# Performance work log

Hardware: AMD Instinct MI355X
Metric: run time of the kernel (lower is better)

## Reference

```python
import jax, jax.numpy as jnp
import numpy as np

D_TOTAL, H, D_HEAD, HID = 2048, 16, 128, 512
EPS = float(np.finfo(np.float32).eps)  # nn.RMSNorm eps=None -> dtype eps


def _xavier(key, shape):
    # xavier_uniform over last two dims (per-head init)
    fan_in, fan_out = shape[-2], shape[-1]
    limit = float(np.sqrt(6.0 / (fan_in + fan_out)))
    return jax.random.uniform(key, shape, jnp.float32, -limit, limit)


def setup_inputs() -> dict:
    key = jax.random.key(0)
    ks = jax.random.split(key, 6)
    x = jax.random.normal(ks[0], (4, 4096, D_TOTAL), jnp.float32)
    g = jnp.ones((D_TOTAL,), jnp.float32)  # RMSNorm weight
    w0 = _xavier(ks[1], (H, D_HEAD, HID))
    w1 = _xavier(ks[2], (H, HID, HID))
    w2 = _xavier(ks[3], (H, HID, HID))
    w3 = _xavier(ks[4], (H, HID, D_HEAD))
    return {"x": x, "g": g, "w0": w0, "w1": w1, "w2": w2, "w3": w3}


def _rms_norm(x, g):
    var = jnp.mean(jnp.square(x), axis=-1, keepdims=True)
    return x * jax.lax.rsqrt(var + EPS) * g


def reference(x, g, w0, w1, w2, w3):
    h = _rms_norm(x, g)
    lead = h.shape[:-1]
    hp = h.reshape(*lead, H, D_HEAD)  # (B,S,H,d_head)
    gelu = lambda t: jax.nn.gelu(t, approximate=False)
    hp = jnp.einsum('bshd,hde->bshe', hp, w0)
    hp = jnp.einsum('bshd,hde->bshe', gelu(hp), w1)
    hp = jnp.einsum('bshd,hde->bshe', gelu(hp), w2)
    hp = jnp.einsum('bshd,hde->bshe', gelu(hp), w3)
    return hp.reshape(*lead, D_TOTAL)
```

## Files before the change

kernel.cpp:

```cpp
#include <hip/hip_runtime.h>
#include <cstdint>
#include <cstddef>

#define N_TOK   16384
#define D_TOTAL 2048
#define N_HEAD  16
#define D_HEAD  128
#define HID     512
#define MT      64
#define RMS_EPS 1.1920929e-07f

typedef __attribute__((ext_vector_type(8))) short  short8;
typedef __attribute__((ext_vector_type(4))) float  float4_t;
typedef __attribute__((ext_vector_type(2))) unsigned int uint2_t;

__device__ __forceinline__ unsigned short f2bf(float f) {
    union { float f; unsigned int i; } v; v.f = f;
    unsigned int b = v.i;
    b += 0x7FFFu + ((b >> 16) & 1u);
    return (unsigned short)(b >> 16);
}

__device__ __forceinline__ unsigned int cvt_pk_bf16(float lo, float hi) {
    unsigned int r;
    asm("v_cvt_pk_bf16_f32 %0, %1, %2" : "=v"(r) : "v"(lo), "v"(hi));
    return r;
}

__device__ __forceinline__ float gelu_exact(float x) {
    float ax = fabsf(x);
    float t  = __builtin_amdgcn_rcpf(fmaf(0.23164193f, ax, 1.0f));
    float poly = fmaf(fmaf(fmaf(fmaf(1.061405429f, t, -1.453152027f),
                               t, 1.421413741f), t, -0.284496736f),
                      t, 0.254829592f) * t;
    float e    = exp2f(x * x * -0.72134752f);
    float erfa = fmaf(-poly, e, 1.0f);
    return fmaf(0.5f * ax, erfa, 0.5f * x);
}

__global__ __launch_bounds__(256) void rms_scale_kernel(
    const float* __restrict__ x, float* __restrict__ scale)
{
    const int lane  = threadIdx.x & 63;
    const int wv    = threadIdx.x >> 6;
    const int token = blockIdx.x * 4 + wv;

    const float* xp = x + (size_t)token * D_TOTAL;
    float s = 0.0f;
#pragma unroll
    for (int j = 0; j < 8; ++j) {
        float4 v = *(const float4*)(xp + (size_t)(j * 64 + lane) * 4);
        s += v.x * v.x + v.y * v.y + v.z * v.z + v.w * v.w;
    }
#pragma unroll
    for (int off = 32; off > 0; off >>= 1) s += __shfl_down(s, off, 64);
    if (lane == 0)
        scale[token] = rsqrtf(s * (1.0f / (float)D_TOTAL) + RMS_EPS);
}

__global__ __launch_bounds__(256) void transpose_kernel(
    const float* __restrict__ in, unsigned short* __restrict__ out, int K, int N,
    const float* __restrict__ gmul)
{
    const int ktiles = K >> 6, ntiles = N >> 6;
    const int b   = blockIdx.x;
    const int h   = b / (ktiles * ntiles);
    const int rem = b % (ktiles * ntiles);
    const int kt  = rem / ntiles, nt = rem % ntiles;

    const float* src = in + (size_t)h * K * N + (size_t)(kt * 64) * N + nt * 64;
    unsigned short* dst = out + (size_t)h * N * K + (size_t)(nt * 64) * K + kt * 64;

    __shared__ unsigned short tile[64][72];

#pragma unroll
    for (int p = 0; p < 2; ++p) {
        int gi = threadIdx.x + p * 256;
        int r  = gi >> 3;
        int gc = (gi & 7) * 8;
        float mul = 1.0f;
        if (gmul) mul = gmul[(size_t)h * K + kt * 64 + r];
        float4 a  = *(const float4*)(src + (size_t)r * N + gc);
        float4 b4 = *(const float4*)(src + (size_t)r * N + gc + 4);
        unsigned short tmp[8];
        tmp[0]=f2bf(a.x*mul);  tmp[1]=f2bf(a.y*mul);  tmp[2]=f2bf(a.z*mul);  tmp[3]=f2bf(a.w*mul);
        tmp[4]=f2bf(b4.x*mul); tmp[5]=f2bf(b4.y*mul); tmp[6]=f2bf(b4.z*mul); tmp[7]=f2bf(b4.w*mul);
        *(uint4*)&tile[r][gc] = *(const uint4*)tmp;
    }
    __syncthreads();
#pragma unroll
    for (int p = 0; p < 2; ++p) {
        int gi  = threadIdx.x + p * 256;
        int r2  = gi >> 3;
        int gc2 = (gi & 7) * 8;
        unsigned short tmp[8];
#pragma unroll
        for (int j = 0; j < 8; ++j) tmp[j] = tile[gc2 + j][r2];
        *(uint4*)(dst + (size_t)r2 * K + gc2) = *(const uint4*)tmp;
    }
}

template<int K, int NT>
__device__ __forceinline__ void stage_gemm(
    const unsigned short* __restrict__ sA,
    const unsigned short* __restrict__ wt,
    int lane, int nbase, float4_t acc[4][NT])
{
#pragma unroll
    for (int mt = 0; mt < 4; ++mt)
#pragma unroll
        for (int nt = 0; nt < NT; ++nt) {
            float4_t z = {0.0f, 0.0f, 0.0f, 0.0f};
            acc[mt][nt] = z;
        }

    const int r15 = lane & 15;
    const int q   = lane >> 4;

    const char* arow[NT];
#pragma unroll
    for (int nt = 0; nt < NT; ++nt)
        arow[nt] = (const char*)(wt + (size_t)(nbase + nt * 16 + r15) * K + q * 8);

    const char* sab = (const char*)sA;
    unsigned int vb[4];
    const unsigned int hb = ((unsigned)(r15 >> 2) & 1u) << 6;
#pragma unroll
    for (int mt = 0; mt < 4; ++mt) {
        unsigned int row = (unsigned)(mt * 16 + r15);
        vb[mt] = row * 1024u + (((unsigned)(q ^ (r15 & 3))) << 4) + hb;
    }

#pragma unroll
    for (int ks = 0; ks < K / 32; ++ks) {
        short8 a[NT], b[4];
#pragma unroll
        for (int nt = 0; nt < NT; ++nt)
            a[nt] = *(const short8*)(arow[nt] + ks * 64);
#pragma unroll
        for (int mt = 0; mt < 4; ++mt)
            b[mt] = *(const short8*)(sab + (vb[mt] ^ (unsigned)(ks * 64)));
#pragma unroll
        for (int mt = 0; mt < 4; ++mt)
#pragma unroll
            for (int nt = 0; nt < NT; ++nt)
                acc[mt][nt] = __builtin_amdgcn_mfma_f32_16x16x32_bf16(
                    a[nt], b[mt], acc[mt][nt], 0, 0, 0);
    }
}

template<int NT>
__device__ __forceinline__ void epi_gelu(
    unsigned short* __restrict__ sAct, int lane, int nbase, float4_t acc[4][NT])
{
    const int q  = lane >> 4;
    const int c0 = lane & 15;
#pragma unroll
    for (int mt = 0; mt < 4; ++mt) {
        const int tok   = mt * 16 + c0;
        const unsigned int rbase = (unsigned)tok * HID;
        const int tk7   = tok & 7;
#pragma unroll
        for (int nt = 0; nt < NT; ++nt) {
            const int col = nbase + nt * 16 + q * 4;
            float g0 = gelu_exact(acc[mt][nt][0]);
            float g1 = gelu_exact(acc[mt][nt][1]);
            float g2 = gelu_exact(acc[mt][nt][2]);
            float g3 = gelu_exact(acc[mt][nt][3]);
            uint2_t v;
            v.x = cvt_pk_bf16(g0, g1);
            v.y = cvt_pk_bf16(g2, g3);
            const int gsw = (col >> 3) ^ tk7;
            *(uint2_t*)&sAct[rbase + gsw * 8 + (col & 7)] = v;
        }
    }
}

__global__ __launch_bounds__(512, 4) void fused_chain_kernel(
    const float*          __restrict__ x,
    const float*          __restrict__ scale,
    const unsigned short* __restrict__ wt0,
    const unsigned short* __restrict__ wt1,
    const unsigned short* __restrict__ wt2,
    const unsigned short* __restrict__ wt3,
    float*                __restrict__ out)
{
    __shared__ unsigned short sAct[MT * HID];

    const int tid  = threadIdx.x;
    const int lane = tid & 63;
    const int wv   = tid >> 6;
    const int bx    = blockIdx.x;
    const int xcd   = bx & 7;
    const int local = bx >> 3;
    const int head  = xcd * 2 + (local >> 8);
    const int tile  = local & 255;
    const int tok0  = tile * MT;

#pragma unroll
    for (int p = 0; p < 2; ++p) {
        int gi = tid + p * 512;
        int r  = gi >> 4;
        int gc = gi & 15;
        int token = tok0 + r;
        const float* xp = x + (size_t)token * D_TOTAL + head * D_HEAD + gc * 8;
        float4 xa = *(const float4*)(xp);
        float4 xb = *(const float4*)(xp + 4);
        float s = scale[token];
        unsigned int u[4];
        u[0] = cvt_pk_bf16(xa.x * s, xa.y * s);
        u[1] = cvt_pk_bf16(xa.z * s, xa.w * s);
        u[2] = cvt_pk_bf16(xb.x * s, xb.y * s);
        u[3] = cvt_pk_bf16(xb.z * s, xb.w * s);
        int gsw = gc ^ (r & 7);
        *(uint4*)&sAct[r * HID + gsw * 8] = *(const uint4*)u;
    }
    __syncthreads();

    float4_t acc[4][4];
    const int nb = wv * 64;

    stage_gemm<128, 4>(sAct, wt0 + (size_t)head * HID * D_HEAD, lane, nb, acc);
    __syncthreads();
    epi_gelu<4>(sAct, lane, nb, acc);
    __syncthreads();

    stage_gemm<512, 4>(sAct, wt1 + (size_t)head * HID * HID, lane, nb, acc);
    __syncthreads();
    epi_gelu<4>(sAct, lane, nb, acc);
    __syncthreads();

    stage_gemm<512, 4>(sAct, wt2 + (size_t)head * HID * HID, lane, nb, acc);
    __syncthreads();
    epi_gelu<4>(sAct, lane, nb, acc);
    __syncthreads();

    float4_t acc2[4][1];
    stage_gemm<512, 1>(sAct, wt3 + (size_t)head * D_HEAD * HID, lane, wv * 16, acc2);

    const int q  = lane >> 4;
    const int c0 = lane & 15;
#pragma unroll
    for (int mt = 0; mt < 4; ++mt) {
        const int token = tok0 + mt * 16 + c0;
        const int col   = head * D_HEAD + wv * 16 + q * 4;
        *(float4_t*)&out[(size_t)token * D_TOTAL + col] = acc2[mt][0];
    }
}

extern "C" void kernel_launch(void* const* d_in, const int* in_sizes, int n_in,
                              void* d_out, int out_size, void* d_ws, size_t ws_size,
                              hipStream_t stream)
{
    const float* x  = (const float*)d_in[0];
    const float* gw = (const float*)d_in[1];
    const float* w0 = (const float*)d_in[2];
    const float* w1 = (const float*)d_in[3];
    const float* w2 = (const float*)d_in[4];
    const float* w3 = (const float*)d_in[5];
    float* out = (float*)d_out;

    float* scale = (float*)d_ws;
    unsigned short* wt0 = (unsigned short*)((char*)d_ws + 65536);
    unsigned short* wt1 = wt0 + (size_t)N_HEAD * HID * D_HEAD;
    unsigned short* wt2 = wt1 + (size_t)N_HEAD * HID * HID;
    unsigned short* wt3 = wt2 + (size_t)N_HEAD * HID * HID;

    rms_scale_kernel<<<N_TOK / 4, 256, 0, stream>>>(x, scale);

    transpose_kernel<<<N_HEAD * (D_HEAD/64) * (HID/64), 256, 0, stream>>>(w0, wt0, D_HEAD, HID, gw);
    transpose_kernel<<<N_HEAD * (HID/64)    * (HID/64), 256, 0, stream>>>(w1, wt1, HID,    HID, nullptr);
    transpose_kernel<<<N_HEAD * (HID/64)    * (HID/64), 256, 0, stream>>>(w2, wt2, HID,    HID, nullptr);
    transpose_kernel<<<N_HEAD * (HID/64)    * (D_HEAD/64), 256, 0, stream>>>(w3, wt3, HID, D_HEAD, nullptr);

    fused_chain_kernel<<<N_HEAD * (N_TOK / MT), 512, 0, stream>>>(
        x, scale, wt0, wt1, wt2, wt3, out);
}
```

Measured before the change: 891.8 us.

## Switch fused MLP chain to 32x32x16 MFMA and merge prep kernels

Replaces the 16x16x32 bf16 MFMA tiling with 32x32x16 MFMA tiles (2x2 per wave) across all four per-head GEMM stages. The LDS swizzle, epilogue and output layout are reworked to match the new fragment shapes. The 32x32 tiles should cut LDS and global fragment loads per FLOP. The RMS-scale kernel and the four weight-transpose kernels are merged into one launch to reduce launch overhead, and the GELU exp2 now uses the hardware builtin. The new swizzle mapping has to match the writer's layout exactly or the results will be wrong.

```diff
diff --git a/kernel.cpp b/kernel.cpp
--- a/kernel.cpp
+++ b/kernel.cpp
@@ -10,9 +10,10 @@
 #define MT      64
 #define RMS_EPS 1.1920929e-07f
 
-typedef __attribute__((ext_vector_type(8))) short  short8;
-typedef __attribute__((ext_vector_type(4))) float  float4_t;
-typedef __attribute__((ext_vector_type(2))) unsigned int uint2_t;
+typedef __attribute__((ext_vector_type(8)))  short  short8;
+typedef __attribute__((ext_vector_type(4)))  float  float4_t;
+typedef __attribute__((ext_vector_type(16))) float  f32x16;
+typedef __attribute__((ext_vector_type(2)))  unsigned int uint2_t;
 
 __device__ __forceinline__ unsigned short f2bf(float f) {
     union { float f; unsigned int i; } v; v.f = f;
@@ -25,6 +26,14 @@
     unsigned int r;
     asm("v_cvt_pk_bf16_f32 %0, %1, %2" : "=v"(r) : "v"(lo), "v"(hi));
     return r;
+}
+
+__device__ __forceinline__ float fast_exp2(float x) {
+#if __has_builtin(__builtin_amdgcn_exp2f)
+    return __builtin_amdgcn_exp2f(x);
+#else
+    return exp2f(x);
+#endif
 }
 
 __device__ __forceinline__ float gelu_exact(float x) {
@@ -33,37 +42,46 @@
     float poly = fmaf(fmaf(fmaf(fmaf(1.061405429f, t, -1.453152027f),
                                t, 1.421413741f), t, -0.284496736f),
                       t, 0.254829592f) * t;
-    float e    = exp2f(x * x * -0.72134752f);
+    float e    = fast_exp2(x * x * -0.72134752f);
     float erfa = fmaf(-poly, e, 1.0f);
     return fmaf(0.5f * ax, erfa, 0.5f * x);
 }
 
-__global__ __launch_bounds__(256) void rms_scale_kernel(
-    const float* __restrict__ x, float* __restrict__ scale)
-{
-    const int lane  = threadIdx.x & 63;
-    const int wv    = threadIdx.x >> 6;
-    const int token = blockIdx.x * 4 + wv;
-
-    const float* xp = x + (size_t)token * D_TOTAL;
-    float s = 0.0f;
-#pragma unroll
-    for (int j = 0; j < 8; ++j) {
-        float4 v = *(const float4*)(xp + (size_t)(j * 64 + lane) * 4);
-        s += v.x * v.x + v.y * v.y + v.z * v.z + v.w * v.w;
-    }
-#pragma unroll
-    for (int off = 32; off > 0; off >>= 1) s += __shfl_down(s, off, 64);
-    if (lane == 0)
-        scale[token] = rsqrtf(s * (1.0f / (float)D_TOTAL) + RMS_EPS);
-}
-
-__global__ __launch_bounds__(256) void transpose_kernel(
-    const float* __restrict__ in, unsigned short* __restrict__ out, int K, int N,
-    const float* __restrict__ gmul)
-{
+__global__ __launch_bounds__(256) void prep_kernel(
+    const float* __restrict__ x, float* __restrict__ scale,
+    const float* __restrict__ w0, const float* __restrict__ w1,
+    const float* __restrict__ w2, const float* __restrict__ w3,
+    const float* __restrict__ gw,
+    unsigned short* __restrict__ wt0, unsigned short* __restrict__ wt1,
+    unsigned short* __restrict__ wt2, unsigned short* __restrict__ wt3)
+{
+    int b = blockIdx.x;
+    if (b < 4096) {
+        const int lane  = threadIdx.x & 63;
+        const int wv    = threadIdx.x >> 6;
+        const int token = b * 4 + wv;
+        const float* xp = x + (size_t)token * D_TOTAL;
+        float s = 0.0f;
+#pragma unroll
+        for (int j = 0; j < 8; ++j) {
+            float4 v = *(const float4*)(xp + (size_t)(j * 64 + lane) * 4);
+            s += v.x * v.x + v.y * v.y + v.z * v.z + v.w * v.w;
+        }
+#pragma unroll
+        for (int off = 32; off > 0; off >>= 1) s += __shfl_down(s, off, 64);
+        if (lane == 0)
+            scale[token] = rsqrtf(s * (1.0f / (float)D_TOTAL) + RMS_EPS);
+        return;
+    }
+
+    b -= 4096;
+    const float* in; unsigned short* out; int K, N; const float* gm = nullptr;
+    if      (b <  256) { in = w0; out = wt0; K = 128; N = 512; gm = gw; }
+    else if (b < 1280) { in = w1; out = wt1; K = 512; N = 512; b -= 256; }
+    else if (b < 2304) { in = w2; out = wt2; K = 512; N = 512; b -= 1280; }
+    else               { in = w3; out = wt3; K = 512; N = 128; b -= 2304; }
+
     const int ktiles = K >> 6, ntiles = N >> 6;
-    const int b   = blockIdx.x;
     const int h   = b / (ktiles * ntiles);
     const int rem = b % (ktiles * ntiles);
     const int kt  = rem / ntiles, nt = rem % ntiles;
@@ -79,7 +97,7 @@
         int r  = gi >> 3;
         int gc = (gi & 7) * 8;
         float mul = 1.0f;
-        if (gmul) mul = gmul[(size_t)h * K + kt * 64 + r];
+        if (gm) mul = gm[(size_t)h * K + kt * 64 + r];
         float4 a  = *(const float4*)(src + (size_t)r * N + gc);
         float4 b4 = *(const float4*)(src + (size_t)r * N + gc + 4);
         unsigned short tmp[8];
@@ -100,79 +118,82 @@
     }
 }
 
-template<int K, int NT>
-__device__ __forceinline__ void stage_gemm(
+template<int K, int MTT, int NT>
+__device__ __forceinline__ void stage_gemm32(
     const unsigned short* __restrict__ sA,
     const unsigned short* __restrict__ wt,
-    int lane, int nbase, float4_t acc[4][NT])
-{
-#pragma unroll
-    for (int mt = 0; mt < 4; ++mt)
-#pragma unroll
-        for (int nt = 0; nt < NT; ++nt) {
-            float4_t z = {0.0f, 0.0f, 0.0f, 0.0f};
-            acc[mt][nt] = z;
-        }
-
-    const int r15 = lane & 15;
-    const int q   = lane >> 4;
+    int lane, int mt0, int nbase, f32x16 acc[MTT][NT])
+{
+#pragma unroll
+    for (int mt = 0; mt < MTT; ++mt)
+#pragma unroll
+        for (int nt = 0; nt < NT; ++nt)
+#pragma unroll
+            for (int i = 0; i < 16; ++i) acc[mt][nt][i] = 0.0f;
+
+    const int r31 = lane & 31;
+    const int h   = lane >> 5;
 
     const char* arow[NT];
 #pragma unroll
     for (int nt = 0; nt < NT; ++nt)
-        arow[nt] = (const char*)(wt + (size_t)(nbase + nt * 16 + r15) * K + q * 8);
+        arow[nt] = (const char*)(wt + (size_t)(nbase + nt * 32 + r31) * K + h * 8);
 
     const char* sab = (const char*)sA;
-    unsigned int vb[4];
-    const unsigned int hb = ((unsigned)(r15 >> 2) & 1u) << 6;
-#pragma unroll
-    for (int mt = 0; mt < 4; ++mt) {
-        unsigned int row = (unsigned)(mt * 16 + r15);
-        vb[mt] = row * 1024u + (((unsigned)(q ^ (r15 & 3))) << 4) + hb;
-    }
-
-#pragma unroll
-    for (int ks = 0; ks < K / 32; ++ks) {
-        short8 a[NT], b[4];
+    unsigned int vb[MTT];
+#pragma unroll
+    for (int mt = 0; mt < MTT; ++mt) {
+        unsigned int row = (unsigned)(mt0 + mt * 32 + r31);
+        unsigned int r7  = row & 7u;
+        unsigned int g0  = (r7 & 6u) | ((unsigned)h ^ (r7 & 1u));
+        vb[mt] = row * 1024u + (g0 << 4);
+    }
+
+#pragma unroll
+    for (int ks = 0; ks < K / 16; ++ks) {
+        short8 a[NT], b[MTT];
 #pragma unroll
         for (int nt = 0; nt < NT; ++nt)
-            a[nt] = *(const short8*)(arow[nt] + ks * 64);
-#pragma unroll
-        for (int mt = 0; mt < 4; ++mt)
-            b[mt] = *(const short8*)(sab + (vb[mt] ^ (unsigned)(ks * 64)));
-#pragma unroll
-        for (int mt = 0; mt < 4; ++mt)
+            a[nt] = *(const short8*)(arow[nt] + ks * 32);
+#pragma unroll
+        for (int mt = 0; mt < MTT; ++mt)
+            b[mt] = *(const short8*)(sab + (vb[mt] ^ (unsigned)(ks << 5)));
+#pragma unroll
+        for (int mt = 0; mt < MTT; ++mt)
 #pragma unroll
             for (int nt = 0; nt < NT; ++nt)
-                acc[mt][nt] = __builtin_amdgcn_mfma_f32_16x16x32_bf16(
+                acc[mt][nt] = __builtin_amdgcn_mfma_f32_32x32x16_bf16(
                     a[nt], b[mt], acc[mt][nt], 0, 0, 0);
     }
 }
 
-template<int NT>
-__device__ __forceinline__ void epi_gelu(
-    unsigned short* __restrict__ sAct, int lane, int nbase, float4_t acc[4][NT])
-{
-    const int q  = lane >> 4;
-    const int c0 = lane & 15;
-#pragma unroll
-    for (int mt = 0; mt < 4; ++mt) {
-        const int tok   = mt * 16 + c0;
+template<int MTT, int NT>
+__device__ __forceinline__ void epi_gelu32(
+    unsigned short* __restrict__ sAct, int lane, int mt0, int nbase,
+    f32x16 acc[MTT][NT])
+{
+    const int r31 = lane & 31;
+    const int h   = lane >> 5;
+#pragma unroll
+    for (int mt = 0; mt < MTT; ++mt) {
+        const int tok = mt0 + mt * 32 + r31;
         const unsigned int rbase = (unsigned)tok * HID;
-        const int tk7   = tok & 7;
-#pragma unroll
-        for (int nt = 0; nt < NT; ++nt) {
-            const int col = nbase + nt * 16 + q * 4;
-            float g0 = gelu_exact(acc[mt][nt][0]);
-            float g1 = gelu_exact(acc[mt][nt][1]);
-            float g2 = gelu_exact(acc[mt][nt][2]);
-            float g3 = gelu_exact(acc[mt][nt][3]);
-            uint2_t v;
-            v.x = cvt_pk_bf16(g0, g1);
-            v.y = cvt_pk_bf16(g2, g3);
-            const int gsw = (col >> 3) ^ tk7;
-            *(uint2_t*)&sAct[rbase + gsw * 8 + (col & 7)] = v;
-        }
+        const int tk7 = tok & 7;
+#pragma unroll
+        for (int nt = 0; nt < NT; ++nt)
+#pragma unroll
+            for (int g = 0; g < 4; ++g) {
+                const int col = nbase + nt * 32 + 8 * g + 4 * h;
+                float g0 = gelu_exact(acc[mt][nt][4 * g + 0]);
+                float g1 = gelu_exact(acc[mt][nt][4 * g + 1]);
+                float g2 = gelu_exact(acc[mt][nt][4 * g + 2]);
+                float g3 = gelu_exact(acc[mt][nt][4 * g + 3]);
+                uint2_t v;
+                v.x = cvt_pk_bf16(g0, g1);
+                v.y = cvt_pk_bf16(g2, g3);
+                const int gsw = (col >> 3) ^ tk7;
+                *(uint2_t*)&sAct[rbase + gsw * 8 + (col & 7)] = v;
+            }
     }
 }
 
@@ -217,34 +238,41 @@
     }
     __syncthreads();
 
-    float4_t acc[4][4];
+    f32x16 acc[2][2];
     const int nb = wv * 64;
 
-    stage_gemm<128, 4>(sAct, wt0 + (size_t)head * HID * D_HEAD, lane, nb, acc);
-    __syncthreads();
-    epi_gelu<4>(sAct, lane, nb, acc);
-    __syncthreads();
-
-    stage_gemm<512, 4>(sAct, wt1 + (size_t)head * HID * HID, lane, nb, acc);
-    __syncthreads();
-    epi_gelu<4>(sAct, lane, nb, acc);
-    __syncthreads();
-
-    stage_gemm<512, 4>(sAct, wt2 + (size_t)head * HID * HID, lane, nb, acc);
-    __syncthreads();
-    epi_gelu<4>(sAct, lane, nb, acc);
-    __syncthreads();
-
-    float4_t acc2[4][1];
-    stage_gemm<512, 1>(sAct, wt3 + (size_t)head * D_HEAD * HID, lane, wv * 16, acc2);
-
-    const int q  = lane >> 4;
-    const int c0 = lane & 15;
-#pragma unroll
-    for (int mt = 0; mt < 4; ++mt) {
-        const int token = tok0 + mt * 16 + c0;
-        const int col   = head * D_HEAD + wv * 16 + q * 4;
-        *(float4_t*)&out[(size_t)token * D_TOTAL + col] = acc2[mt][0];
+    stage_gemm32<128, 2, 2>(sAct, wt0 + (size_t)head * HID * D_HEAD, lane, 0, nb, acc);
+    __syncthreads();
+    epi_gelu32<2, 2>(sAct, lane, 0, nb, acc);
+    __syncthreads();
+
+    stage_gemm32<512, 2, 2>(sAct, wt1 + (size_t)head * HID * HID, lane, 0, nb, acc);
+    __syncthreads();
+    epi_gelu32<2, 2>(sAct, lane, 0, nb, acc);
+    __syncthreads();
+
+    stage_gemm32<512, 2, 2>(sAct, wt2 + (size_t)head * HID * HID, lane, 0, nb, acc);
+    __syncthreads();
+    epi_gelu32<2, 2>(sAct, lane, 0, nb, acc);
+    __syncthreads();
+
+    const int mt4 = (wv >> 2) * 32;
+    const int nt4 = (wv & 3) * 32;
+    f32x16 acc2[1][1];
+    stage_gemm32<512, 1, 1>(sAct, wt3 + (size_t)head * D_HEAD * HID, lane, mt4, nt4, acc2);
+
+    const int r31 = lane & 31;
+    const int h   = lane >> 5;
+    const int token = tok0 + mt4 + r31;
+#pragma unroll
+    for (int g = 0; g < 4; ++g) {
+        const int col = head * D_HEAD + nt4 + 8 * g + 4 * h;
+        float4_t v;
+        v[0] = acc2[0][0][4 * g + 0];
+        v[1] = acc2[0][0][4 * g + 1];
+        v[2] = acc2[0][0][4 * g + 2];
+        v[3] = acc2[0][0][4 * g + 3];
+        *(float4_t*)&out[(size_t)token * D_TOTAL + col] = v;
     }
 }
 
@@ -266,12 +294,8 @@
     unsigned short* wt2 = wt1 + (size_t)N_HEAD * HID * HID;
     unsigned short* wt3 = wt2 + (size_t)N_HEAD * HID * HID;
 
-    rms_scale_kernel<<<N_TOK / 4, 256, 0, stream>>>(x, scale);
-
-    transpose_kernel<<<N_HEAD * (D_HEAD/64) * (HID/64), 256, 0, stream>>>(w0, wt0, D_HEAD, HID, gw);
-    transpose_kernel<<<N_HEAD * (HID/64)    * (HID/64), 256, 0, stream>>>(w1, wt1, HID,    HID, nullptr);
-    transpose_kernel<<<N_HEAD * (HID/64)    * (HID/64), 256, 0, stream>>>(w2, wt2, HID,    HID, nullptr);
-    transpose_kernel<<<N_HEAD * (HID/64)    * (D_HEAD/64), 256, 0, stream>>>(w3, wt3, HID, D_HEAD, nullptr);
+    prep_kernel<<<4096 + 2560, 256, 0, stream>>>(
+        x, scale, w0, w1, w2, w3, gw, wt0, wt1, wt2, wt3);
 
     fused_chain_kernel<<<N_HEAD * (N_TOK / MT), 512, 0, stream>>>(
         x, scale, wt0, wt1, wt2, wt3, out);
```

Result: slower. 933.6 us (+4.7%).
